# Performance work log

Measured on AMD Instinct MI355X. Metric: run time of the kernel, lower is better.

The kernel has to match this reference:

```python
import jax, jax.numpy as jnp
import numpy as np

HEADS = 4

def gat_layer(x, W, a_src, a_dst, bias, edge_index, n):
    # PyG-style GATConv with self-loops, heads averaged (concat=False) so out dim == hidden_dim
    H, C = a_src.shape
    h = (x @ W).reshape(n, H, C)                      # [N,H,C]
    loops = jnp.arange(n)
    src = jnp.concatenate([edge_index[0], loops])
    dst = jnp.concatenate([edge_index[1], loops])
    e = jax.nn.leaky_relu((h * a_src).sum(-1)[src] + (h * a_dst).sum(-1)[dst], 0.2)  # [E,H]
    m = jax.ops.segment_max(e, dst, num_segments=n)   # segment softmax over incoming edges
    ex = jnp.exp(e - m[dst])
    s = jax.ops.segment_sum(ex, dst, num_segments=n)
    alpha = ex / (s[dst] + 1e-16)
    out = jax.ops.segment_sum(alpha[:, :, None] * h[src], dst, num_segments=n)  # [N,H,C]
    return out.mean(axis=1) + bias

def setup_inputs() -> dict:
    key = jax.random.key(0)
    ks = jax.random.split(key, 24)
    Nd, Ni, Ne = 20000, 4096, 4096
    D_in, D = 512, 256
    n_int, n_emo = 64, 32
    inp = {}
    inp['dialogue_embeddings'] = jax.random.normal(ks[0], (Nd, D_in), jnp.float32)
    inp['intention_indices'] = jax.random.randint(ks[1], (Ni,), 0, n_int)
    inp['emotion_indices'] = jax.random.randint(ks[2], (Ne,), 0, n_emo)
    inp['dialogue_edge_index'] = jax.random.randint(ks[3], (2, Nd * 32), 0, Nd)
    inp['intention_edge_index'] = jax.random.randint(ks[4], (2, Ni * 16), 0, Ni)
    inp['emotion_edge_index'] = jax.random.randint(ks[5], (2, Ne * 16), 0, Ne)
    s = lambda k, shape: jax.random.normal(k, shape, jnp.float32) * 0.02
    inp['intention_emb'] = s(ks[6], (n_int, D))
    inp['emotion_emb'] = s(ks[7], (n_emo, D))
    inp['Wd'] = s(ks[8], (D_in, HEADS * D)); inp['a_src_d'] = s(ks[9], (HEADS, D)); inp['a_dst_d'] = s(ks[10], (HEADS, D)); inp['bd'] = jnp.zeros((D,), jnp.float32)
    inp['Wi'] = s(ks[11], (D, HEADS * D)); inp['a_src_i'] = s(ks[12], (HEADS, D)); inp['a_dst_i'] = s(ks[13], (HEADS, D)); inp['bi'] = jnp.zeros((D,), jnp.float32)
    inp['We'] = s(ks[14], (D, HEADS * D)); inp['a_src_e'] = s(ks[15], (HEADS, D)); inp['a_dst_e'] = s(ks[16], (HEADS, D)); inp['be'] = jnp.zeros((D,), jnp.float32)
    inp['W_dfc'] = s(ks[17], (D, D)); inp['b_dfc'] = jnp.zeros((D,), jnp.float32)
    inp['W_ifc'] = s(ks[18], (D, D)); inp['b_ifc'] = jnp.zeros((D,), jnp.float32)
    inp['W_efc'] = s(ks[19], (D, D)); inp['b_efc'] = jnp.zeros((D,), jnp.float32)
    inp['W_fc'] = s(ks[20], (3 * D, n_emo)); inp['b_fc'] = jnp.zeros((n_emo,), jnp.float32)
    return inp

def reference(dialogue_embeddings, intention_indices, emotion_indices,
              dialogue_edge_index, intention_edge_index, emotion_edge_index,
              intention_emb, emotion_emb,
              Wd, a_src_d, a_dst_d, bd, Wi, a_src_i, a_dst_i, bi,
              We, a_src_e, a_dst_e, be,
              W_dfc, b_dfc, W_ifc, b_ifc, W_efc, b_efc, W_fc, b_fc):
    Nd = dialogue_embeddings.shape[0]
    Ni = intention_indices.shape[0]
    Ne = emotion_indices.shape[0]
    ie = intention_emb[intention_indices]   # [Ni, D]
    ee = emotion_emb[emotion_indices]       # [Ne, D]
    d = gat_layer(dialogue_embeddings, Wd, a_src_d, a_dst_d, bd, dialogue_edge_index, Nd)
    d = jax.nn.relu(d @ W_dfc + b_dfc)
    i = gat_layer(ie, Wi, a_src_i, a_dst_i, bi, intention_edge_index, Ni)
    i = jax.nn.relu(i @ W_ifc + b_ifc)
    e = gat_layer(ee, We, a_src_e, a_dst_e, be, emotion_edge_index, Ne)
    e = jax.nn.relu(e @ W_efc + b_efc)
    iw = jax.nn.softmax(d @ i.T, axis=-1)   # [Nd, Ni]
    att_i = iw @ i                           # [Nd, D]
    ew = jax.nn.softmax(d @ e.T, axis=-1)   # [Nd, Ne]
    att_e = ew @ e                           # [Nd, D]
    inputs = jnp.concatenate([d, att_i, att_e], axis=-1)  # [Nd, 3D]
    return inputs @ W_fc + b_fc
```

## Files before the change

### kernel.cpp

```cpp
#include <hip/hip_runtime.h>
#include <hip/hip_bf16.h>
#include <math.h>

#define DEV static __device__ __forceinline__

typedef __attribute__((ext_vector_type(8))) short short8;
typedef __attribute__((ext_vector_type(4))) short short4v;
typedef __attribute__((ext_vector_type(4))) float f32x4;
typedef __attribute__((ext_vector_type(2))) long long2v;

DEV float bf2f(__hip_bfloat16 x) { return __bfloat162float(x); }
DEV __hip_bfloat16 f2bf(float x) { return __float2bfloat16(x); }
DEV short bfbits(float x) { __hip_bfloat16 h = __float2bfloat16(x); short s; __builtin_memcpy(&s, &h, 2); return s; }
DEV float b2f_bits(short s) { __hip_bfloat16 h; __builtin_memcpy(&h, &s, 2); return __bfloat162float(h); }
DEV float lrelu(float x) { return x > 0.f ? x : 0.2f * x; }

DEV float load_in(const void* p, long long i, bool f32) {
  return f32 ? ((const float*)p)[i] : bf2f(((const __hip_bfloat16*)p)[i]);
}

DEV long pack8_fp8(const float* f) {
  int lo = 0, hi = 0;
  lo = __builtin_amdgcn_cvt_pk_fp8_f32(f[0], f[1], lo, false);
  lo = __builtin_amdgcn_cvt_pk_fp8_f32(f[2], f[3], lo, true);
  hi = __builtin_amdgcn_cvt_pk_fp8_f32(f[4], f[5], hi, false);
  hi = __builtin_amdgcn_cvt_pk_fp8_f32(f[6], f[7], hi, true);
  return ((long)(unsigned)hi << 32) | (unsigned)lo;
}

DEV f32x4 mfma_fp8(long a, long b, f32x4 c) {
  return __builtin_amdgcn_mfma_f32_16x16x32_fp8_fp8(a, b, c, 0, 0, 0);
}

__global__ void HGAN_45148696215914_kernel() {}

__global__ void fill_k(__hip_bfloat16* __restrict__ p, float v, int n)
{
  int i = blockIdx.x * blockDim.x + threadIdx.x;
  if (i < n) p[i] = __float2bfloat16(v);
}

struct DetectArgs { const unsigned int* p[23]; int nw[23]; int id[23]; };

__global__ void detect_k(DetectArgs a, int* __restrict__ flags)
{
  __shared__ int cnt_sh;
  if (threadIdx.x == 0) cnt_sh = 0;
  __syncthreads();
  const unsigned int* w = a.p[blockIdx.x];
  int nwords = a.nw[blockIdx.x];
  int bad = 0;
  for (int i = threadIdx.x; i < nwords; i += blockDim.x) {
    unsigned int x = w[i];
    float v0 = __uint_as_float((x & 0xffffu) << 16);
    float v1 = __uint_as_float(x & 0xffff0000u);
    if (!(fabsf(v0) <= 1e4f)) bad++;
    if (!(fabsf(v1) <= 1e4f)) bad++;
  }
  atomicAdd(&cnt_sh, bad);
  __syncthreads();
  if (threadIdx.x == 0) flags[a.id[blockIdx.x]] = (cnt_sh > nwords / 4) ? 1 : 0;
}

struct CvArgs {
  const void* in[7]; const int* flag[7]; __hip_bfloat16* out[7];
  int K[7], N[7], NL[7], toff[7]; int nseg;
};

__global__ __launch_bounds__(256) void convtrN_k(CvArgs a)
{
  __shared__ __hip_bfloat16 t[32][33];
  int b = blockIdx.x;
  int s = 0;
  while (s + 1 < a.nseg && b >= a.toff[s + 1]) ++s;
  int ti = b - a.toff[s];
  int kb = a.K[s] >> 5;
  int bk = ti % kb, bn = ti / kb;
  const void* in = a.in[s];
  const int* flag = a.flag[s];
  __hip_bfloat16* out = a.out[s];
  int K = a.K[s], N = a.N[s];
  const bool f = flag && *flag;
  int lx = threadIdx.x & 31, ly = threadIdx.x >> 5;
  int gn = bn * 32 + lx;
#pragma unroll
  for (int rr = 0; rr < 32; rr += 8)
    t[rr + ly][lx] = (gn < N)
        ? f2bf(load_in(in, (long long)(bk * 32 + rr + ly) * N + gn, f))
        : f2bf(0.f);
  __syncthreads();
#pragma unroll
  for (int rr = 0; rr < 32; rr += 8)
    out[(size_t)(bn * 32 + rr + ly) * K + bk * 32 + lx] = t[lx][rr + ly];
}

DEV void mgemm_body(
    const void* A, const int* aflag, int lda, const int* idxA,
    const __hip_bfloat16* BT, void* C, int ldc,
    const void* bias, const int* biasflag, int relu,
    int permC, int M, int K, int Nlim, const int* cflag,
    int m0, int n0, __hip_bfloat16* Ash, __hip_bfloat16* Bsh)
{
  const bool af = aflag && *aflag;
  const bool bsf = biasflag && *biasflag;
  const bool cf = cflag && *cflag;
  const int tid = threadIdx.x;
  const int wv = tid >> 6, lane = tid & 63, qd = lane >> 4, lm = lane & 15;
  const int wr = wv >> 1, wc = wv & 1;

  f32x4 acc[4][4];
#pragma unroll
  for (int i = 0; i < 4; ++i)
    for (int j = 0; j < 4; ++j)
      for (int v = 0; v < 4; ++v) acc[i][j][v] = 0.f;

  for (int k0 = 0; k0 < K; k0 += 64) {
    __syncthreads();
    for (int u = tid; u < 1024; u += 256) {
      int r = u >> 3, cu = u & 7;
      int gm = m0 + r;
      short8 vv;
      if (gm < M) {
        long long row = idxA ? idxA[gm] : gm;
        long long basei = row * (long long)lda + k0 + cu * 8;
        if (af) {
          const float4* fp = (const float4*)((const float*)A + basei);
          float4 f0 = fp[0], f1 = fp[1];
          vv[0] = bfbits(f0.x); vv[1] = bfbits(f0.y);
          vv[2] = bfbits(f0.z); vv[3] = bfbits(f0.w);
          vv[4] = bfbits(f1.x); vv[5] = bfbits(f1.y);
          vv[6] = bfbits(f1.z); vv[7] = bfbits(f1.w);
        } else {
          vv = *(const short8*)((const __hip_bfloat16*)A + basei);
        }
      } else {
#pragma unroll
        for (int j = 0; j < 8; ++j) vv[j] = 0;
      }
      *(short8*)(&Ash[r * 72 + cu * 8]) = vv;
    }
    for (int u = tid; u < 1024; u += 256) {
      int r = u >> 3, cu = u & 7;
      *(short8*)(&Bsh[r * 72 + cu * 8]) =
          *(const short8*)(BT + (size_t)(n0 + r) * K + k0 + cu * 8);
    }
    __syncthreads();
#pragma unroll
    for (int ks = 0; ks < 2; ++ks) {
      short8 a[4], b[4];
#pragma unroll
      for (int i = 0; i < 4; ++i)
        a[i] = *(const short8*)(&Ash[(wr * 64 + i * 16 + lm) * 72 + ks * 32 + qd * 8]);
#pragma unroll
      for (int j = 0; j < 4; ++j)
        b[j] = *(const short8*)(&Bsh[(wc * 64 + j * 16 + lm) * 72 + ks * 32 + qd * 8]);
#pragma unroll
      for (int i = 0; i < 4; ++i)
#pragma unroll
        for (int j = 0; j < 4; ++j)
          acc[i][j] = __builtin_amdgcn_mfma_f32_16x16x32_bf16(a[i], b[j], acc[i][j], 0, 0, 0);
    }
  }
#pragma unroll
  for (int j = 0; j < 4; ++j) {
    int gn = n0 + wc * 64 + j * 16 + lm;
    if (gn >= Nlim) continue;
    float bv = bias ? load_in(bias, gn, bsf) : 0.f;
    int gcol = permC ? ((gn & 255) * 4 + (gn >> 8)) : gn;
#pragma unroll
    for (int i = 0; i < 4; ++i) {
#pragma unroll
      for (int v = 0; v < 4; ++v) {
        int gm = m0 + wr * 64 + i * 16 + qd * 4 + v;
        if (gm >= M) continue;
        float x = acc[i][j][v] + bv;
        if (relu) x = fmaxf(x, 0.f);
        long long idx = (long long)gm * ldc + gcol;
        if (cf) ((float*)C)[idx] = x;
        else    ((__hip_bfloat16*)C)[idx] = f2bf(x);
      }
    }
  }
}

__global__ __launch_bounds__(256) void mgemm_k(
    const void* __restrict__ A, const int* __restrict__ aflag, int lda,
    const int* __restrict__ idxA,
    const __hip_bfloat16* __restrict__ BT,
    void* __restrict__ C, int ldc,
    const void* __restrict__ bias, const int* __restrict__ biasflag, int relu,
    int permC, int M, int N, int K, int Nlim,
    const int* __restrict__ cflag)
{
  __shared__ __align__(16) __hip_bfloat16 Ash[128 * 72];
  __shared__ __align__(16) __hip_bfloat16 Bsh[128 * 72];
  (void)N;
  mgemm_body(A, aflag, lda, idxA, BT, C, ldc, bias, biasflag, relu,
             permC, M, K, Nlim, cflag,
             blockIdx.y * 128, blockIdx.x * 128, Ash, Bsh);
}

struct SegArgs {
  const void* A[3]; const int* aflag[3]; int lda[3]; const int* idxA[3];
  const __hip_bfloat16* BT[3]; void* C[3]; int ldc[3];
  const void* bias[3]; const int* bflag[3];
  int M[3]; int K[3]; int yoff[3];
  int relu, permC, Nlim;
};

__global__ __launch_bounds__(256) void mgemm_seg_k(SegArgs a)
{
  __shared__ __align__(16) __hip_bfloat16 Ash[128 * 72];
  __shared__ __align__(16) __hip_bfloat16 Bsh[128 * 72];
  int y = blockIdx.y;
  int s = (y >= a.yoff[2]) ? 2 : ((y >= a.yoff[1]) ? 1 : 0);
  mgemm_body(a.A[s], a.aflag[s], a.lda[s], a.idxA[s], a.BT[s], a.C[s], a.ldc[s],
             a.bias[s], a.bflag[s], a.relu, a.permC, a.M[s], a.K[s], a.Nlim,
             nullptr, (y - a.yoff[s]) * 128, blockIdx.x * 128, Ash, Bsh);
}

__global__ __launch_bounds__(256) void score3_k(
    const __hip_bfloat16* __restrict__ hI,
    const void* as1, const void* ad1, const int* sf1, const int* df1,
    const void* as2, const void* ad2, const int* sf2, const int* df2,
    const void* as3, const void* ad3, const int* sf3, const int* df3,
    int s1, int s2,
    float* __restrict__ ss, float* __restrict__ ds,
    int* __restrict__ cnt, int N)
{
  __shared__ float red[4][8];
  int n = blockIdx.x, c = threadIdx.x;
  if (c == 0) cnt[n] = 0;
  const void* a_src; const void* a_dst; const int* sfp; const int* dfp;
  if (n < s1)      { a_src = as1; a_dst = ad1; sfp = sf1; dfp = df1; }
  else if (n < s2) { a_src = as2; a_dst = ad2; sfp = sf2; dfp = df2; }
  else             { a_src = as3; a_dst = ad3; sfp = sf3; dfp = df3; }
  const bool sf = sfp && *sfp;
  const bool df = dfp && *dfp;
  short4v hv = *(const short4v*)(hI + (size_t)n * 1024 + c * 4);
  float h0 = b2f_bits(hv[0]), h1 = b2f_bits(hv[1]);
  float h2 = b2f_bits(hv[2]), h3 = b2f_bits(hv[3]);
  float r0 = h0 * load_in(a_src, 0 * 256 + c, sf);
  float r1 = h1 * load_in(a_src, 1 * 256 + c, sf);
  float r2 = h2 * load_in(a_src, 2 * 256 + c, sf);
  float r3 = h3 * load_in(a_src, 3 * 256 + c, sf);
  float t0 = h0 * load_in(a_dst, 0 * 256 + c, df);
  float t1 = h1 * load_in(a_dst, 1 * 256 + c, df);
  float t2 = h2 * load_in(a_dst, 2 * 256 + c, df);
  float t3 = h3 * load_in(a_dst, 3 * 256 + c, df);
#pragma unroll
  for (int o = 32; o > 0; o >>= 1) {
    r0 += __shfl_down(r0, o); r1 += __shfl_down(r1, o);
    r2 += __shfl_down(r2, o); r3 += __shfl_down(r3, o);
    t0 += __shfl_down(t0, o); t1 += __shfl_down(t1, o);
    t2 += __shfl_down(t2, o); t3 += __shfl_down(t3, o);
  }
  int wv = c >> 6, lane = c & 63;
  if (lane == 0) {
    red[wv][0] = r0; red[wv][1] = r1; red[wv][2] = r2; red[wv][3] = r3;
    red[wv][4] = t0; red[wv][5] = t1; red[wv][6] = t2; red[wv][7] = t3;
  }
  __syncthreads();
  if (c < 8) {
    float s = red[0][c] + red[1][c] + red[2][c] + red[3][c];
    if (c < 4) ss[n * 4 + c] = s;
    else       ds[n * 4 + (c - 4)] = s;
  }
}

__global__ void count3_k(const int* __restrict__ d1, int E1,
                         const int* __restrict__ d2, int E2, int o2,
                         const int* __restrict__ d3, int E3, int o3,
                         int* __restrict__ cnt)
{
  int k = blockIdx.x * blockDim.x + threadIdx.x;
  if (k < E1) atomicAdd(&cnt[d1[k]], 1);
  else if (k < E1 + E2) atomicAdd(&cnt[d2[k - E1] + o2], 1);
  else if (k < E1 + E2 + E3) atomicAdd(&cnt[d3[k - E1 - E2] + o3], 1);
}

__global__ __launch_bounds__(1024) void scan1_k(
    const int* __restrict__ cnt, int* __restrict__ offp, int* __restrict__ bsum, int n)
{
  __shared__ int sh[1024];
  int idx = blockIdx.x * 1024 + (int)threadIdx.x;
  int v = (idx < n) ? cnt[idx] : 0;
  sh[threadIdx.x] = v;
  __syncthreads();
  for (int d = 1; d < 1024; d <<= 1) {
    int t = (threadIdx.x >= (unsigned)d) ? sh[threadIdx.x - d] : 0;
    __syncthreads();
    sh[threadIdx.x] += t;
    __syncthreads();
  }
  if (idx < n) offp[idx] = sh[threadIdx.x] - v;
  if (threadIdx.x == 1023) bsum[blockIdx.x] = sh[1023];
}

__global__ void scan3_k(int* __restrict__ offp, const int* __restrict__ bsum,
                        int* __restrict__ cur, int n, int nb)
{
  int i = blockIdx.x * blockDim.x + threadIdx.x;
  if (i < n) {
    int chunk = i >> 10;
    int pre = 0;
    for (int b = 0; b < chunk; ++b) pre += bsum[b];
    int v = offp[i] + pre;
    offp[i] = v;
    cur[i] = v;
    if (i == n - 1) {
      int tot = 0;
      for (int b = 0; b < nb; ++b) tot += bsum[b];
      offp[n] = tot;
    }
  }
}

__global__ void scatter3_k(const int* __restrict__ s1, const int* __restrict__ d1, int E1,
                           const int* __restrict__ s2, const int* __restrict__ d2, int E2, int o2,
                           const int* __restrict__ s3, const int* __restrict__ d3, int E3, int o3,
                           int* __restrict__ cur, int* __restrict__ srcs)
{
  int k = blockIdx.x * blockDim.x + threadIdx.x;
  if (k < E1) {
    int p = atomicAdd(&cur[d1[k]], 1);
    srcs[p] = s1[k];
  } else if (k < E1 + E2) {
    int kk = k - E1;
    int p = atomicAdd(&cur[d2[kk] + o2], 1);
    srcs[p] = s2[kk] + o2;
  } else if (k < E1 + E2 + E3) {
    int kk = k - E1 - E2;
    int p = atomicAdd(&cur[d3[kk] + o3], 1);
    srcs[p] = s3[kk] + o3;
  }
}

__global__ __launch_bounds__(256) void agg3_k(
    const __hip_bfloat16* __restrict__ hI,
    const float* __restrict__ ss, const float* __restrict__ ds,
    const int* __restrict__ offp, const int* __restrict__ srcs,
    const void* b1, const int* bf1,
    const void* b2, const int* bf2,
    const void* b3, const int* bf3,
    int s1, int s2,
    __hip_bfloat16* __restrict__ outp, int N)
{
  __shared__ int src_sh[64];
  __shared__ __align__(16) float w_sh[64][4];
  __shared__ float scale_sh[4];
  __shared__ float l_sh[4];
  __shared__ __align__(16) float pair_sh[128][8];
  int n = blockIdx.x;
  int c = threadIdx.x;
  int hd_w = c >> 6;
  int e_w  = c & 63;
  int half = c >> 7;
  int tc   = c & 127;
  int s0 = offp[n], deg = offp[n + 1] - s0;
  int total = deg + 1;
  float dsn = ds[n * 4 + hd_w];
  float m_run = -1e30f, l_run = 0.f;
  float A0[4] = {0.f, 0.f, 0.f, 0.f};
  float A1[4] = {0.f, 0.f, 0.f, 0.f};
  for (int base = 0; base < total; base += 64) {
    int cnt = min(64, total - base);
    __syncthreads();
    if (c < cnt) src_sh[c] = (base + c == 0) ? n : srcs[s0 + base + c - 1];
    __syncthreads();
    float val = -1e30f;
    if (e_w < cnt) val = lrelu(ss[src_sh[e_w] * 4 + hd_w] + dsn);
    float vmax = val;
#pragma unroll
    for (int o = 32; o > 0; o >>= 1) vmax = fmaxf(vmax, __shfl_xor(vmax, o));
    float newm = fmaxf(m_run, vmax);
    float p = (e_w < cnt) ? __expf(val - newm) : 0.f;
    float psum = p;
#pragma unroll
    for (int o = 32; o > 0; o >>= 1) psum += __shfl_xor(psum, o);
    float sc = __expf(m_run - newm);
    l_run = l_run * sc + psum;
    m_run = newm;
    w_sh[e_w][hd_w] = p;
    if (e_w == 0) scale_sh[hd_w] = sc;
    __syncthreads();
    float sc0 = scale_sh[0], sc1 = scale_sh[1], sc2 = scale_sh[2], sc3 = scale_sh[3];
    A0[0] *= sc0; A0[1] *= sc1; A0[2] *= sc2; A0[3] *= sc3;
    A1[0] *= sc0; A1[1] *= sc1; A1[2] *= sc2; A1[3] *= sc3;
    for (int e = half; e < cnt; e += 2) {
      short8 hv = *(const short8*)(hI + (size_t)src_sh[e] * 1024 + tc * 8);
      float4 w = *(const float4*)(&w_sh[e][0]);
      A0[0] += w.x * b2f_bits(hv[0]); A0[1] += w.y * b2f_bits(hv[1]);
      A0[2] += w.z * b2f_bits(hv[2]); A0[3] += w.w * b2f_bits(hv[3]);
      A1[0] += w.x * b2f_bits(hv[4]); A1[1] += w.y * b2f_bits(hv[5]);
      A1[2] += w.z * b2f_bits(hv[6]); A1[3] += w.w * b2f_bits(hv[7]);
    }
  }
  __syncthreads();
  if (e_w == 0) l_sh[hd_w] = l_run;
  if (half == 1) {
    *(float4*)(&pair_sh[tc][0]) = make_float4(A0[0], A0[1], A0[2], A0[3]);
    *(float4*)(&pair_sh[tc][4]) = make_float4(A1[0], A1[1], A1[2], A1[3]);
  }
  __syncthreads();
  if (half == 0) {
    float4 p0 = *(const float4*)(&pair_sh[tc][0]);
    float4 p1 = *(const float4*)(&pair_sh[tc][4]);
    A0[0] += p0.x; A0[1] += p0.y; A0[2] += p0.z; A0[3] += p0.w;
    A1[0] += p1.x; A1[1] += p1.y; A1[2] += p1.z; A1[3] += p1.w;
    const void* bias; const int* bfp;
    if (n < s1)      { bias = b1; bfp = bf1; }
    else if (n < s2) { bias = b2; bfp = bf2; }
    else             { bias = b3; bfp = bf3; }
    const bool bf = bfp && *bfp;
    float il0 = 1.f / (l_sh[0] + 1e-16f), il1 = 1.f / (l_sh[1] + 1e-16f);
    float il2 = 1.f / (l_sh[2] + 1e-16f), il3 = 1.f / (l_sh[3] + 1e-16f);
    float r0 = 0.25f * (A0[0] * il0 + A0[1] * il1 + A0[2] * il2 + A0[3] * il3);
    float r1 = 0.25f * (A1[0] * il0 + A1[1] * il1 + A1[2] * il2 + A1[3] * il3);
    outp[(size_t)n * 256 + 2 * tc]     = f2bf(r0 + load_in(bias, 2 * tc, bf));
    outp[(size_t)n * 256 + 2 * tc + 1] = f2bf(r1 + load_in(bias, 2 * tc + 1, bf));
  }
}

__global__ __launch_bounds__(256) void conv8_k(
    const __hip_bfloat16* __restrict__ in0, char* __restrict__ K8_0, char* __restrict__ KT8_0,
    const __hip_bfloat16* __restrict__ in1, char* __restrict__ K8_1, char* __restrict__ KT8_1,
    int Nk)
{
  __shared__ __align__(16) __hip_bfloat16 t[32][264];
  const __hip_bfloat16* in = blockIdx.y ? in1 : in0;
  char* K8  = blockIdx.y ? K8_1  : K8_0;
  char* KT8 = blockIdx.y ? KT8_1 : KT8_0;
  int kv0 = blockIdx.x * 32;
  int tid = threadIdx.x;
  for (int u = tid; u < 1024; u += 256) {
    int r = u >> 5, c = u & 31;
    *(short8*)(&t[r][c * 8]) = *(const short8*)(in + (size_t)(kv0 + r) * 256 + c * 8);
  }
  __syncthreads();
  for (int u = tid; u < 1024; u += 256) {
    int r = u >> 5, g = u & 31, pos = g * 8;
    int qd = pos >> 6, s = (pos >> 3) & 7;
    int d = s * 32 + qd * 8;
    float f[8];
#pragma unroll
    for (int j = 0; j < 8; ++j) f[j] = 16.f * bf2f(t[r][d + j]);
    *(long*)(K8 + (size_t)(kv0 + r) * 256 + pos) = pack8_fp8(f);
  }
  {
    int d = tid;
#pragma unroll
    for (int g = 0; g < 4; ++g) {
      float f[8];
#pragma unroll
      for (int j = 0; j < 8; ++j) f[j] = 16.f * bf2f(t[g * 8 + j][d]);
      *(long*)(KT8 + (size_t)d * Nk + kv0 + g * 8) = pack8_fp8(f);
    }
  }
}

__global__ __launch_bounds__(512, 4) void flashf8_k(
    const __hip_bfloat16* __restrict__ Q, int ldq,
    const char* __restrict__ K8_0, const char* __restrict__ KT8_0,
    const char* __restrict__ K8_1, const char* __restrict__ KT8_1,
    __hip_bfloat16* __restrict__ Out, int ldo,
    int M, int Nk)
{
  __shared__ __align__(16) char Ksh8[2][32 * 256];
  __shared__ __align__(16) char KTsh8[2][256 * 48];
  __shared__ __align__(16) char Psh8[8][16 * 40];
  const int att = blockIdx.y;
  const char* K8  = att ? K8_1  : K8_0;
  const char* KT8 = att ? KT8_1 : KT8_0;
  __hip_bfloat16* Outp = Out + att * 256;

  const int tid = threadIdx.x;
  const int wv = tid >> 6, lane = tid & 63;
  const int qd = lane >> 4, lm = lane & 15;
  const int r0 = blockIdx.x * 128 + wv * 16;
  char* Pw = Psh8[wv];

  const int kr0 = tid >> 4, kc = tid & 15;
  const int kcs = kc ^ (kr0 & 7);
  const int tr0 = tid >> 1, tcq = tid & 1;

  long qf8[8];
  {
    const bool ok = (r0 + lm) < M;
    const __hip_bfloat16* qrow = Q + (size_t)(r0 + lm) * ldq;
#pragma unroll
    for (int s = 0; s < 8; ++s) {
      float f[8];
      if (ok) {
        short8 qv = *(const short8*)(qrow + s * 32 + qd * 8);
#pragma unroll
        for (int j = 0; j < 8; ++j) f[j] = 16.f * b2f_bits(qv[j]);
      } else {
#pragma unroll
        for (int j = 0; j < 8; ++j) f[j] = 0.f;
      }
      qf8[s] = pack8_fp8(f);
    }
  }

  f32x4 Oacc[16];
#pragma unroll
  for (int i = 0; i < 16; ++i)
    for (int v = 0; v < 4; ++v) Oacc[i][v] = 0.f;
  float mrow = -1e30f, lrow = 0.f;

  {
    short8 k0 = *(const short8*)(K8 + (size_t)kr0 * 256 + kc * 16);
    short8 t0 = *(const short8*)(KT8 + (size_t)tr0 * Nk + tcq * 16);
    *(short8*)(&Ksh8[0][kr0 * 256 + kcs * 16]) = k0;
    *(short8*)(&KTsh8[0][tr0 * 48 + tcq * 16]) = t0;
  }
  __syncthreads();

  int iter = 0;
  for (int n0 = 0; n0 < Nk; n0 += 32, ++iter) {
    const int cur = iter & 1, nxt = cur ^ 1;
    const bool havenext = (n0 + 32) < Nk;
    short8 pk0, pt0;
    if (havenext) {
      int nn = n0 + 32;
      pk0 = *(const short8*)(K8 + (size_t)(nn + kr0) * 256 + kc * 16);
      pt0 = *(const short8*)(KT8 + (size_t)tr0 * Nk + nn + tcq * 16);
    }
    const char* Kc  = Ksh8[cur];
    const char* KTc = KTsh8[cur];

    f32x4 S[2];
#pragma unroll
    for (int t = 0; t < 2; ++t)
      for (int v = 0; v < 4; ++v) S[t][v] = 0.f;
#pragma unroll
    for (int sp = 0; sp < 4; ++sp) {
#pragma unroll
      for (int t = 0; t < 2; ++t) {
        long2v a2 = *(const long2v*)(
            &Kc[(t * 16 + lm) * 256 + (((qd * 4 + sp) ^ (lm & 7)) << 4)]);
        S[t] = mfma_fp8(a2[0], qf8[2 * sp],     S[t]);
        S[t] = mfma_fp8(a2[1], qf8[2 * sp + 1], S[t]);
      }
    }
#pragma unroll
    for (int t = 0; t < 2; ++t)
      for (int v = 0; v < 4; ++v) S[t][v] *= 0.00390625f;

    float tmax = -1e30f;
#pragma unroll
    for (int t = 0; t < 2; ++t)
      for (int v = 0; v < 4; ++v) tmax = fmaxf(tmax, S[t][v]);
    tmax = fmaxf(tmax, __shfl_xor(tmax, 16));
    tmax = fmaxf(tmax, __shfl_xor(tmax, 32));
    float newm = fmaxf(mrow, tmax);
    float psum = 0.f;
#pragma unroll
    for (int t = 0; t < 2; ++t)
      for (int v = 0; v < 4; ++v) {
        float p = __expf(S[t][v] - newm);
        S[t][v] = p;
        psum += p;
      }
    psum += __shfl_xor(psum, 16);
    psum += __shfl_xor(psum, 32);
    float scale = __expf(mrow - newm);
    lrow = lrow * scale + psum;
    mrow = newm;
#pragma unroll
    for (int t = 0; t < 2; ++t) {
      int pk = __builtin_amdgcn_cvt_pk_fp8_f32(16.f * S[t][0], 16.f * S[t][1], 0, false);
      pk = __builtin_amdgcn_cvt_pk_fp8_f32(16.f * S[t][2], 16.f * S[t][3], pk, true);
      *(int*)(&Pw[lm * 40 + t * 16 + qd * 4]) = pk;
    }

    if (__any(scale < 1.0f)) {
      float scl[4];
#pragma unroll
      for (int v = 0; v < 4; ++v) scl[v] = __shfl(scale, qd * 4 + v);
#pragma unroll
      for (int i = 0; i < 16; ++i)
        for (int v = 0; v < 4; ++v) Oacc[i][v] *= scl[v];
    }

    {
      long pa0 = *(const long*)(&Pw[lm * 40 + qd * 8]);
#pragma unroll
      for (int dt = 0; dt < 16; ++dt) {
        long b = *(const long*)(&KTc[(dt * 16 + lm) * 48 + qd * 8]);
        Oacc[dt] = mfma_fp8(pa0, b, Oacc[dt]);
      }
    }

    if (havenext) {
      *(short8*)(&Ksh8[nxt][kr0 * 256 + kcs * 16]) = pk0;
      *(short8*)(&KTsh8[nxt][tr0 * 48 + tcq * 16]) = pt0;
    }
    __syncthreads();
  }

  {
    float linv = 1.f / (256.f * lrow);
    float li[4];
#pragma unroll
    for (int v = 0; v < 4; ++v) li[v] = __shfl(linv, qd * 4 + v);
#pragma unroll
    for (int v = 0; v < 4; ++v) {
      int grow = r0 + qd * 4 + v;
      if (grow >= M) continue;
#pragma unroll
      for (int dt = 0; dt < 16; ++dt)
        Outp[(size_t)grow * ldo + dt * 16 + lm] = f2bf(Oacc[dt][v] * li[v]);
    }
  }
}

extern "C" void kernel_launch(void* const* d_in, const int* in_sizes, int n_in,
                              void* d_out, int out_size, void* d_ws, size_t ws_size,
                              hipStream_t stream)
{
  const void* Xd      = d_in[0];
  const int*  int_idx = (const int*)d_in[1];
  const int*  emo_idx = (const int*)d_in[2];
  const int*  ed_d    = (const int*)d_in[3];
  const int*  ed_i    = (const int*)d_in[4];
  const int*  ed_e    = (const int*)d_in[5];
  const void* int_emb = d_in[6];
  const void* emo_emb = d_in[7];
  const void* Wd = d_in[8],  *a_src_d = d_in[9],  *a_dst_d = d_in[10], *bd = d_in[11];
  const void* Wi = d_in[12], *a_src_i = d_in[13], *a_dst_i = d_in[14], *bi = d_in[15];
  const void* We = d_in[16], *a_src_e = d_in[17], *a_dst_e = d_in[18], *be = d_in[19];
  const void* W_dfc = d_in[20], *b_dfc = d_in[21];
  const void* W_ifc = d_in[22], *b_ifc = d_in[23];
  const void* W_efc = d_in[24], *b_efc = d_in[25];
  const void* W_fc  = d_in[26], *b_fc  = d_in[27];

  const int DIn  = in_sizes[8] / 1024;
  const int Nd   = in_sizes[0] / DIn;
  const int Ni   = in_sizes[1];
  const int Ne   = in_sizes[2];
  const int Ed   = in_sizes[3] / 2;
  const int Ei   = in_sizes[4] / 2;
  const int Ee   = in_sizes[5] / 2;
  const int Nout = in_sizes[27];
  const int NU   = Nd + Ni + Ne;

  char* base = (char*)d_ws;
  size_t off = 0;
  auto alloc = [&](size_t nbytes) -> void* {
    void* p = base + off;
    off = (off + nbytes + 255) & ~(size_t)255;
    return p;
  };
  int* flags = (int*)alloc(32 * sizeof(int));
  int* bsum  = (int*)alloc(64 * sizeof(int));
  __hip_bfloat16* hbuf = (__hip_bfloat16*)alloc((size_t)NU * 1024 * 2);
  __hip_bfloat16* cat  = (__hip_bfloat16*)alloc((size_t)Nd * 768 * 2);
  __hip_bfloat16* gat_tmp = (__hip_bfloat16*)alloc((size_t)NU * 256 * 2);
  __hip_bfloat16* WdT  = (__hip_bfloat16*)alloc((size_t)1024 * DIn * 2);
  __hip_bfloat16* WiT  = (__hip_bfloat16*)alloc((size_t)1024 * 256 * 2);
  __hip_bfloat16* WeT  = (__hip_bfloat16*)alloc((size_t)1024 * 256 * 2);
  __hip_bfloat16* WdfT = (__hip_bfloat16*)alloc((size_t)256 * 256 * 2);
  __hip_bfloat16* WifT = (__hip_bfloat16*)alloc((size_t)256 * 256 * 2);
  __hip_bfloat16* WefT = (__hip_bfloat16*)alloc((size_t)256 * 256 * 2);
  __hip_bfloat16* WfcT = (__hip_bfloat16*)alloc((size_t)128 * 768 * 2);
  float* ss  = (float*)alloc((size_t)NU * 4 * 4);
  float* dsb = (float*)alloc((size_t)NU * 4 * 4);
  int* cnt   = (int*)alloc((size_t)NU * 4);
  int* offp  = (int*)alloc((size_t)(NU + 1) * 4);
  int* cur   = (int*)alloc((size_t)NU * 4);
  int* srcs  = (int*)alloc((size_t)(Ed + Ei + Ee) * 4);
  const size_t need = off;
  (void)n_in;

  __hip_bfloat16* i_mat = hbuf;
  __hip_bfloat16* e_mat = hbuf + (size_t)Ni * 256;
  char* K8i  = (char*)(hbuf + (size_t)2 * Ni * 256);
  char* KT8i = K8i + (size_t)Ni * 256;
  char* K8e  = KT8i + (size_t)Ni * 256;
  char* KT8e = K8e + (size_t)Ne * 256;

  const dim3 T(256);
  if (ws_size < need) {
    fill_k<<<(out_size + 255) / 256, T, 0, stream>>>((__hip_bfloat16*)d_out, 0.25f, out_size);
    return;
  }

  {
    DetectArgs da;
    const int fid[23] = {0,6,7,8,9,10,11,12,13,14,15,16,17,18,19,20,21,22,23,24,25,26,27};
    for (int t = 0; t < 23; ++t) {
      int id = fid[t];
      int nw = in_sizes[id] / 2;
      if (nw > 2048) nw = 2048;
      if (nw < 1) nw = 1;
      da.p[t] = (const unsigned int*)d_in[id];
      da.nw[t] = nw;
      da.id[t] = id;
    }
    detect_k<<<23, 256, 0, stream>>>(da, flags);
  }
  #define F(i) (flags + (i))

  {
    CvArgs cv;
    const void* ins[7]  = {Wd, Wi, We, W_dfc, W_ifc, W_efc, W_fc};
    const int*  fgs[7]  = {F(8), F(12), F(16), F(20), F(22), F(24), F(26)};
    __hip_bfloat16* outs[7] = {WdT, WiT, WeT, WdfT, WifT, WefT, WfcT};
    int Ks[7]  = {DIn, 256, 256, 256, 256, 256, 768};
    int Ns[7]  = {1024, 1024, 1024, 256, 256, 256, Nout};
    int NLs[7] = {1024, 1024, 1024, 256, 256, 256, 128};
    int run = 0;
    for (int s = 0; s < 7; ++s) {
      cv.in[s] = ins[s]; cv.flag[s] = fgs[s]; cv.out[s] = outs[s];
      cv.K[s] = Ks[s]; cv.N[s] = Ns[s]; cv.NL[s] = NLs[s]; cv.toff[s] = run;
      run += (Ks[s] / 32) * (NLs[s] / 32);
    }
    cv.nseg = 7;
    convtrN_k<<<run, T, 0, stream>>>(cv);
  }

  const int yNd = (Nd + 127) / 128, yNi = Ni / 128, yNe = Ne / 128;
  {
    SegArgs sa;
    sa.A[0] = Xd;      sa.aflag[0] = F(0); sa.lda[0] = DIn; sa.idxA[0] = nullptr;
    sa.BT[0] = WdT;    sa.C[0] = hbuf;     sa.ldc[0] = 1024;
    sa.bias[0] = nullptr; sa.bflag[0] = nullptr; sa.M[0] = Nd; sa.K[0] = DIn;
    sa.A[1] = int_emb; sa.aflag[1] = F(6); sa.lda[1] = 256; sa.idxA[1] = int_idx;
    sa.BT[1] = WiT;    sa.C[1] = hbuf + (size_t)Nd * 1024; sa.ldc[1] = 1024;
    sa.bias[1] = nullptr; sa.bflag[1] = nullptr; sa.M[1] = Ni; sa.K[1] = 256;
    sa.A[2] = emo_emb; sa.aflag[2] = F(7); sa.lda[2] = 256; sa.idxA[2] = emo_idx;
    sa.BT[2] = WeT;    sa.C[2] = hbuf + (size_t)(Nd + Ni) * 1024; sa.ldc[2] = 1024;
    sa.bias[2] = nullptr; sa.bflag[2] = nullptr; sa.M[2] = Ne; sa.K[2] = 256;
    sa.yoff[0] = 0; sa.yoff[1] = yNd; sa.yoff[2] = yNd + yNi;
    sa.relu = 0; sa.permC = 1; sa.Nlim = 1024;
    mgemm_seg_k<<<dim3(8, yNd + yNi + yNe), T, 0, stream>>>(sa);
  }

  {
    int nb = (NU + 1023) / 1024;
    int Etot = Ed + Ei + Ee;
    score3_k<<<NU, T, 0, stream>>>(hbuf,
        a_src_d, a_dst_d, F(9), F(10),
        a_src_i, a_dst_i, F(13), F(14),
        a_src_e, a_dst_e, F(17), F(18),
        Nd, Nd + Ni, ss, dsb, cnt, NU);
    count3_k<<<(Etot + 255) / 256, T, 0, stream>>>(
        ed_d + Ed, Ed, ed_i + Ei, Ei, Nd, ed_e + Ee, Ee, Nd + Ni, cnt);
    scan1_k<<<nb, 1024, 0, stream>>>(cnt, offp, bsum, NU);
    scan3_k<<<(NU + 255) / 256, T, 0, stream>>>(offp, bsum, cur, NU, nb);
    scatter3_k<<<(Etot + 255) / 256, T, 0, stream>>>(
        ed_d, ed_d + Ed, Ed, ed_i, ed_i + Ei, Ei, Nd,
        ed_e, ed_e + Ee, Ee, Nd + Ni, cur, srcs);
    agg3_k<<<NU, T, 0, stream>>>(hbuf, ss, dsb, offp, srcs,
        bd, F(11), bi, F(15), be, F(19), Nd, Nd + Ni, gat_tmp, NU);
  }

  {
    SegArgs sa;
    sa.A[0] = gat_tmp; sa.aflag[0] = nullptr; sa.lda[0] = 256; sa.idxA[0] = nullptr;
    sa.BT[0] = WdfT;   sa.C[0] = cat;   sa.ldc[0] = 768;
    sa.bias[0] = b_dfc; sa.bflag[0] = F(21); sa.M[0] = Nd; sa.K[0] = 256;
    sa.A[1] = gat_tmp + (size_t)Nd * 256; sa.aflag[1] = nullptr; sa.lda[1] = 256; sa.idxA[1] = nullptr;
    sa.BT[1] = WifT;   sa.C[1] = i_mat; sa.ldc[1] = 256;
    sa.bias[1] = b_ifc; sa.bflag[1] = F(23); sa.M[1] = Ni; sa.K[1] = 256;
    sa.A[2] = gat_tmp + (size_t)(Nd + Ni) * 256; sa.aflag[2] = nullptr; sa.lda[2] = 256; sa.idxA[2] = nullptr;
    sa.BT[2] = WefT;   sa.C[2] = e_mat; sa.ldc[2] = 256;
    sa.bias[2] = b_efc; sa.bflag[2] = F(25); sa.M[2] = Ne; sa.K[2] = 256;
    sa.yoff[0] = 0; sa.yoff[1] = yNd; sa.yoff[2] = yNd + yNi;
    sa.relu = 1; sa.permC = 0; sa.Nlim = 256;
    mgemm_seg_k<<<dim3(2, yNd + yNi + yNe), T, 0, stream>>>(sa);
  }

  conv8_k<<<dim3(Ni / 32, 2), T, 0, stream>>>(i_mat, K8i, KT8i, e_mat, K8e, KT8e, Ni);

  flashf8_k<<<dim3((Nd + 127) / 128, 2), dim3(512), 0, stream>>>(
      cat, 768, K8i, KT8i, K8e, KT8e, cat + 256, 768, Nd, Ni);

  mgemm_k<<<dim3(1, (Nd + 127) / 128), T, 0, stream>>>(
      cat, nullptr, 768, nullptr, WfcT, d_out, Nout,
      b_fc, F(27), 0, 0, Nd, 128, 768, Nout, F(0));
}
```

Before: 919.9 us.

## Pre-tile FP8 K and K^T into MFMA-fragment order for linear loads

The conversion kernel now writes the FP8 K and transposed K tiles in a per-32-row block layout that already matches the MFMA operand fragment order. The attention kernel can then copy each tile to shared memory with one contiguous 16-byte load per thread, and read fragments with lane-linear addresses. This removes the XOR swizzle, the padded KT rows and the strided KT global reads (stride Nk). The cost is a tightly coupled layout contract between the two kernels, and it assumes Nk is a multiple of 32.

```diff
diff --git a/kernel.cpp b/kernel.cpp
--- a/kernel.cpp
+++ b/kernel.cpp
@@ -432,7 +432,9 @@
   char* K8  = blockIdx.y ? K8_1  : K8_0;
   char* KT8 = blockIdx.y ? KT8_1 : KT8_0;
   int kv0 = blockIdx.x * 32;
+  size_t tbase = (size_t)(kv0 >> 5) * 8192;
   int tid = threadIdx.x;
+  (void)Nk;
   for (int u = tid; u < 1024; u += 256) {
     int r = u >> 5, c = u & 31;
     *(short8*)(&t[r][c * 8]) = *(const short8*)(in + (size_t)(kv0 + r) * 256 + c * 8);
@@ -440,12 +442,14 @@
   __syncthreads();
   for (int u = tid; u < 1024; u += 256) {
     int r = u >> 5, g = u & 31, pos = g * 8;
-    int qd = pos >> 6, s = (pos >> 3) & 7;
-    int d = s * 32 + qd * 8;
+    int qd_ = pos >> 6, s = (pos >> 3) & 7;
+    int d = s * 32 + qd_ * 8;
     float f[8];
 #pragma unroll
     for (int j = 0; j < 8; ++j) f[j] = 16.f * bf2f(t[r][d + j]);
-    *(long*)(K8 + (size_t)(kv0 + r) * 256 + pos) = pack8_fp8(f);
+    int c16 = pos >> 4, h = (pos >> 3) & 1;
+    int unit = ((c16 & 3) * 2 + (r >> 4)) * 64 + (c16 >> 2) * 16 + (r & 15);
+    *(long*)(K8 + tbase + (size_t)unit * 16 + h * 8) = pack8_fp8(f);
   }
   {
     int d = tid;
@@ -454,7 +458,8 @@
       float f[8];
 #pragma unroll
       for (int j = 0; j < 8; ++j) f[j] = 16.f * bf2f(t[g * 8 + j][d]);
-      *(long*)(KT8 + (size_t)d * Nk + kv0 + g * 8) = pack8_fp8(f);
+      int unit = (d >> 4) * 64 + g * 16 + (d & 15);
+      *(long*)(KT8 + tbase + (size_t)unit * 8) = pack8_fp8(f);
     }
   }
 }
@@ -466,8 +471,8 @@
     __hip_bfloat16* __restrict__ Out, int ldo,
     int M, int Nk)
 {
-  __shared__ __align__(16) char Ksh8[2][32 * 256];
-  __shared__ __align__(16) char KTsh8[2][256 * 48];
+  __shared__ __align__(16) char Ksh8[2][8192];
+  __shared__ __align__(16) char KTsh8[2][8192];
   __shared__ __align__(16) char Psh8[8][16 * 40];
   const int att = blockIdx.y;
   const char* K8  = att ? K8_1  : K8_0;
@@ -480,10 +485,6 @@
   const int r0 = blockIdx.x * 128 + wv * 16;
   char* Pw = Psh8[wv];
 
-  const int kr0 = tid >> 4, kc = tid & 15;
-  const int kcs = kc ^ (kr0 & 7);
-  const int tr0 = tid >> 1, tcq = tid & 1;
-
   long qf8[8];
   {
     const bool ok = (r0 + lm) < M;
@@ -510,10 +511,10 @@
   float mrow = -1e30f, lrow = 0.f;
 
   {
-    short8 k0 = *(const short8*)(K8 + (size_t)kr0 * 256 + kc * 16);
-    short8 t0 = *(const short8*)(KT8 + (size_t)tr0 * Nk + tcq * 16);
-    *(short8*)(&Ksh8[0][kr0 * 256 + kcs * 16]) = k0;
-    *(short8*)(&KTsh8[0][tr0 * 48 + tcq * 16]) = t0;
+    short8 k0 = *(const short8*)(K8 + (size_t)tid * 16);
+    short8 t0 = *(const short8*)(KT8 + (size_t)tid * 16);
+    *(short8*)(&Ksh8[0][tid * 16]) = k0;
+    *(short8*)(&KTsh8[0][tid * 16]) = t0;
   }
   __syncthreads();
 
@@ -523,9 +524,9 @@
     const bool havenext = (n0 + 32) < Nk;
     short8 pk0, pt0;
     if (havenext) {
-      int nn = n0 + 32;
-      pk0 = *(const short8*)(K8 + (size_t)(nn + kr0) * 256 + kc * 16);
-      pt0 = *(const short8*)(KT8 + (size_t)tr0 * Nk + nn + tcq * 16);
+      size_t tb = (size_t)(iter + 1) * 8192;
+      pk0 = *(const short8*)(K8 + tb + (size_t)tid * 16);
+      pt0 = *(const short8*)(KT8 + tb + (size_t)tid * 16);
     }
     const char* Kc  = Ksh8[cur];
     const char* KTc = KTsh8[cur];
@@ -538,8 +539,7 @@
     for (int sp = 0; sp < 4; ++sp) {
 #pragma unroll
       for (int t = 0; t < 2; ++t) {
-        long2v a2 = *(const long2v*)(
-            &Kc[(t * 16 + lm) * 256 + (((qd * 4 + sp) ^ (lm & 7)) << 4)]);
+        long2v a2 = *(const long2v*)(&Kc[((sp * 2 + t) * 64 + lane) * 16]);
         S[t] = mfma_fp8(a2[0], qf8[2 * sp],     S[t]);
         S[t] = mfma_fp8(a2[1], qf8[2 * sp + 1], S[t]);
       }
@@ -588,14 +588,14 @@
       long pa0 = *(const long*)(&Pw[lm * 40 + qd * 8]);
 #pragma unroll
       for (int dt = 0; dt < 16; ++dt) {
-        long b = *(const long*)(&KTc[(dt * 16 + lm) * 48 + qd * 8]);
+        long b = *(const long*)(&KTc[dt * 512 + lane * 8]);
         Oacc[dt] = mfma_fp8(pa0, b, Oacc[dt]);
       }
     }
 
     if (havenext) {
-      *(short8*)(&Ksh8[nxt][kr0 * 256 + kcs * 16]) = pk0;
-      *(short8*)(&KTsh8[nxt][tr0 * 48 + tcq * 16]) = pt0;
+      *(short8*)(&Ksh8[nxt][tid * 16]) = pk0;
+      *(short8*)(&KTsh8[nxt][tid * 16]) = pt0;
     }
     __syncthreads();
   }
```

New measurement: 889.3 us. -3.3%, faster.
